# Optimization experiments

Measured on AMD Instinct MI355X. Metric: run time of the kernel, lower is better.

The kernel has to match this reference:

```python
import jax, jax.numpy as jnp
import numpy as np

N_NODES = 100000
N_EDGES = 1600000
N_GRAPHS = 512
IN_F, HID, OUT_F = 50, 128, 4


def _linear_params(key, fan_in, fan_out, bias=True):
    k1, k2 = jax.random.split(key)
    bound = 1.0 / np.sqrt(fan_in)
    W = jax.random.uniform(k1, (fan_out, fan_in), minval=-bound, maxval=bound, dtype=jnp.float32)
    if bias:
        b = jax.random.uniform(k2, (fan_out,), minval=-bound, maxval=bound, dtype=jnp.float32)
        return W, b
    return W, None


def setup_inputs() -> dict:
    key = jax.random.key(0)
    ks = jax.random.split(key, 12)
    x = jax.random.normal(ks[0], (N_NODES, IN_F), dtype=jnp.float32)
    edge_index = jax.random.randint(ks[1], (2, N_EDGES), 0, N_NODES, dtype=jnp.int32)
    batch = jnp.sort(jax.random.randint(ks[2], (N_NODES,), 0, N_GRAPHS, dtype=jnp.int32))
    # GraphConv params: lin_rel (with bias) applied to aggregated msgs, lin_root (no bias)
    W_rel1, b_rel1 = _linear_params(ks[3], IN_F, HID)
    W_root1, _ = _linear_params(ks[4], IN_F, HID, bias=False)
    W_rel2, b_rel2 = _linear_params(ks[5], HID, HID)
    W_root2, _ = _linear_params(ks[6], HID, HID, bias=False)
    W_rel3, b_rel3 = _linear_params(ks[7], HID, HID)
    W_root3, _ = _linear_params(ks[8], HID, HID, bias=False)
    W_lin, b_lin = _linear_params(ks[9], HID, OUT_F)
    return dict(x=x, edge_index=edge_index, batch=batch,
                W_rel1=W_rel1, b_rel1=b_rel1, W_root1=W_root1,
                W_rel2=W_rel2, b_rel2=b_rel2, W_root2=W_root2,
                W_rel3=W_rel3, b_rel3=b_rel3, W_root3=W_root3,
                W_lin=W_lin, b_lin=b_lin)


def _graph_conv(x, src, dst, W_rel, b_rel, W_root):
    # sum-aggregate neighbor features into target nodes, then two linears
    agg = jax.ops.segment_sum(x[src], dst, num_segments=N_NODES)  # [N, F_in]
    return agg @ W_rel.T + b_rel + x @ W_root.T


def reference(x, edge_index, batch,
              W_rel1, b_rel1, W_root1,
              W_rel2, b_rel2, W_root2,
              W_rel3, b_rel3, W_root3,
              W_lin, b_lin):
    src, dst = edge_index[0], edge_index[1]
    h = jax.nn.relu(_graph_conv(x, src, dst, W_rel1, b_rel1, W_root1))
    h = jax.nn.relu(_graph_conv(h, src, dst, W_rel2, b_rel2, W_root2))
    h = _graph_conv(h, src, dst, W_rel3, b_rel3, W_root3)
    # global mean pool over graphs
    sums = jax.ops.segment_sum(h, batch, num_segments=N_GRAPHS)  # [G, HID]
    counts = jax.ops.segment_sum(jnp.ones((N_NODES,), h.dtype), batch, num_segments=N_GRAPHS)
    pooled = sums / jnp.maximum(counts, 1.0)[:, None]
    # dropout is identity in eval mode
    return pooled @ W_lin.T + b_lin
```

## Files before the change

### kernel.cpp

```cpp
#include <hip/hip_runtime.h>
#include <hip/hip_bf16.h>
#include <stdint.h>

#define N_NODES 100000
#define N_EDGES 1600000
#define N_GRAPHS 512
#define IN_F 50
#define HID 128

#define NPART 8
#define PART_NODES ((N_NODES + NPART - 1) / NPART)

typedef __attribute__((ext_vector_type(8))) short bf16x8;
typedef __attribute__((ext_vector_type(4))) float f32x4;

__device__ __forceinline__ float bf2f(unsigned short s) {
    return __uint_as_float(((unsigned)s) << 16);
}
__device__ __forceinline__ unsigned short f2bf(float f) {
    unsigned u = __float_as_uint(f);
    u = (u + 0x7FFFu + ((u >> 16) & 1u)) >> 16;
    return (unsigned short)u;
}

#define PREP_W2 (N_NODES * 64)
#define PREP_W0 N_NODES
#define PREP_W1 (128 * 64 + 128 * 128)
#define PREP_W3 (N_GRAPHS + 1)
#define PREP_TOTAL (PREP_W2 + PREP_W0 + PREP_W1 + PREP_W3)

__global__ __launch_bounds__(256) void prep_all(
    const float* __restrict__ x, unsigned short* __restrict__ xbf,
    int* __restrict__ deg,
    const float* __restrict__ Wr1, const float* __restrict__ Wo1,
    const float* __restrict__ Wr2, const float* __restrict__ Wo2,
    const float* __restrict__ Wr3, const float* __restrict__ Wo3,
    unsigned short* __restrict__ o_r1, unsigned short* __restrict__ o_o1,
    unsigned short* __restrict__ o_r2, unsigned short* __restrict__ o_o2,
    unsigned short* __restrict__ o_r3, unsigned short* __restrict__ o_o3,
    const int* __restrict__ batch, int* __restrict__ gstart) {
    int idx = blockIdx.x * 256 + threadIdx.x;
    if (idx < PREP_W2) {
        int n = idx >> 6, c = idx & 63;
        float v = (c < IN_F) ? x[(size_t)n * IN_F + c] : 0.f;
        xbf[idx] = f2bf(v);
        return;
    }
    idx -= PREP_W2;
    if (idx < PREP_W0) { deg[idx] = 0; return; }
    idx -= PREP_W0;
    if (idx < PREP_W1) {
        if (idx < 128 * 64) {
            int n = idx >> 6, k = idx & 63;
            unsigned short a = 0, b = 0;
            if (k < IN_F) { a = f2bf(Wr1[n * IN_F + k]); b = f2bf(Wo1[n * IN_F + k]); }
            o_r1[idx] = a; o_o1[idx] = b;
        } else {
            int i2 = idx - 128 * 64;
            o_r2[i2] = f2bf(Wr2[i2]); o_o2[i2] = f2bf(Wo2[i2]);
            o_r3[i2] = f2bf(Wr3[i2]); o_o3[i2] = f2bf(Wo3[i2]);
        }
        return;
    }
    idx -= PREP_W1;
    if (idx < PREP_W3) {
        if (idx == N_GRAPHS) { gstart[idx] = N_NODES; return; }
        int lo = 0, hi = N_NODES;
        while (lo < hi) { int m = (lo + hi) >> 1; if (batch[m] < idx) lo = m + 1; else hi = m; }
        gstart[idx] = lo;
    }
}

__global__ __launch_bounds__(256) void deg_hist(const int* __restrict__ dst,
                                                int* __restrict__ deg) {
    int part = blockIdx.x & (NPART - 1);
    int plo = part * PART_NODES, phi = plo + PART_NODES;
    int base = (blockIdx.x >> 3) * 256 + threadIdx.x;
    int stride = (gridDim.x >> 3) * 256;
    for (int e = base; e < N_EDGES; e += stride) {
        int d = dst[e];
        if (d >= plo && d < phi) atomicAdd(&deg[d], 1);
    }
}

__global__ __launch_bounds__(256) void csr_fill(const int* __restrict__ src,
                                                const int* __restrict__ dst,
                                                int* __restrict__ cursor,
                                                int* __restrict__ csr_src) {
    int part = blockIdx.x & (NPART - 1);
    int plo = part * PART_NODES, phi = plo + PART_NODES;
    int base = (blockIdx.x >> 3) * 256 + threadIdx.x;
    int stride = (gridDim.x >> 3) * 256;
    for (int e = base; e < N_EDGES; e += stride) {
        int d = dst[e];
        if (d >= plo && d < phi) {
            int p = atomicAdd(&cursor[d], 1);
            csr_src[p] = src[e];
        }
    }
}

#define SCAN_BLOCKS ((N_NODES + 1023) / 1024)

__global__ __launch_bounds__(256) void scan_phase1(const int* __restrict__ deg,
                                                   int* __restrict__ blocksum) {
    __shared__ int red[256];
    int b = blockIdx.x, t = threadIdx.x;
    int base = b * 1024 + t * 4;
    int s = 0;
#pragma unroll
    for (int i = 0; i < 4; i++) { int idx = base + i; if (idx < N_NODES) s += deg[idx]; }
    red[t] = s;
    __syncthreads();
    for (int off = 128; off > 0; off >>= 1) {
        if (t < off) red[t] += red[t + off];
        __syncthreads();
    }
    if (t == 0) blocksum[b] = red[0];
}

__global__ __launch_bounds__(128) void scan_phase2(const int* __restrict__ blocksum,
                                                   int* __restrict__ blockoff) {
    __shared__ int v[SCAN_BLOCKS];
    int t = threadIdx.x;
    if (t < SCAN_BLOCKS) v[t] = blocksum[t];
    __syncthreads();
    if (t == 0) {
        int run = 0;
        for (int i = 0; i < SCAN_BLOCKS; i++) { blockoff[i] = run; run += v[i]; }
        blockoff[SCAN_BLOCKS] = run;
    }
}

__global__ __launch_bounds__(256) void scan_phase3(const int* __restrict__ deg,
                                                   const int* __restrict__ blockoff,
                                                   int* __restrict__ rowptr,
                                                   int* __restrict__ cursor) {
    __shared__ int red[256];
    int b = blockIdx.x, t = threadIdx.x;
    int base = b * 1024 + t * 4;
    int e[4];
    int s = 0;
#pragma unroll
    for (int i = 0; i < 4; i++) {
        int idx = base + i;
        e[i] = (idx < N_NODES) ? deg[idx] : 0;
        s += e[i];
    }
    red[t] = s;
    __syncthreads();
    for (int off = 1; off < 256; off <<= 1) {
        int u = (t >= off) ? red[t - off] : 0;
        __syncthreads();
        red[t] += u;
        __syncthreads();
    }
    int prefix = red[t] - s + blockoff[b];
#pragma unroll
    for (int i = 0; i < 4; i++) {
        int idx = base + i;
        if (idx < N_NODES) { rowptr[idx] = prefix; cursor[idx] = prefix; prefix += e[i]; }
    }
    if (b == 0 && t == 0) rowptr[N_NODES] = blockoff[SCAN_BLOCKS];
}

__global__ __launch_bounds__(256) void gather_x64(const unsigned short* __restrict__ xbf,
                                                  const int* __restrict__ rowptr,
                                                  const int* __restrict__ csr_src,
                                                  unsigned short* __restrict__ aggbf) {
    int gid = blockIdx.x * 256 + threadIdx.x;
    int n = gid >> 4;
    int c = threadIdx.x & 15;
    if (n >= N_NODES) return;
    int jb = rowptr[n], je = rowptr[n + 1];
    const uint2* hu = reinterpret_cast<const uint2*>(xbf);
    float a0 = 0.f, a1 = 0.f, a2 = 0.f, a3 = 0.f;
    int j = jb;
    for (; j + 3 < je; j += 4) {
        int s0 = csr_src[j], s1 = csr_src[j + 1], s2 = csr_src[j + 2], s3 = csr_src[j + 3];
        uint2 v0 = hu[(size_t)s0 * 16 + c];
        uint2 v1 = hu[(size_t)s1 * 16 + c];
        uint2 v2 = hu[(size_t)s2 * 16 + c];
        uint2 v3 = hu[(size_t)s3 * 16 + c];
        a0 += (bf2f(v0.x & 0xFFFF) + bf2f(v1.x & 0xFFFF)) + (bf2f(v2.x & 0xFFFF) + bf2f(v3.x & 0xFFFF));
        a1 += (bf2f(v0.x >> 16) + bf2f(v1.x >> 16)) + (bf2f(v2.x >> 16) + bf2f(v3.x >> 16));
        a2 += (bf2f(v0.y & 0xFFFF) + bf2f(v1.y & 0xFFFF)) + (bf2f(v2.y & 0xFFFF) + bf2f(v3.y & 0xFFFF));
        a3 += (bf2f(v0.y >> 16) + bf2f(v1.y >> 16)) + (bf2f(v2.y >> 16) + bf2f(v3.y >> 16));
    }
    for (; j < je; j++) {
        int s0 = csr_src[j];
        uint2 v0 = hu[(size_t)s0 * 16 + c];
        a0 += bf2f(v0.x & 0xFFFF);
        a1 += bf2f(v0.x >> 16);
        a2 += bf2f(v0.y & 0xFFFF);
        a3 += bf2f(v0.y >> 16);
    }
    uint2 pk;
    pk.x = (unsigned)f2bf(a0) | ((unsigned)f2bf(a1) << 16);
    pk.y = (unsigned)f2bf(a2) | ((unsigned)f2bf(a3) << 16);
    reinterpret_cast<uint2*>(aggbf)[(size_t)n * 16 + c] = pk;
}

__global__ __launch_bounds__(256) void gather_bf128(const unsigned short* __restrict__ h,
                                                    const int* __restrict__ rowptr,
                                                    const int* __restrict__ csr_src,
                                                    unsigned short* __restrict__ aggbf) {
    int gid = blockIdx.x * 256 + threadIdx.x;
    int n = gid >> 5;
    int c = threadIdx.x & 31;
    if (n >= N_NODES) return;
    int jb = rowptr[n], je = rowptr[n + 1];
    const uint2* hu = reinterpret_cast<const uint2*>(h);
    float a0 = 0.f, a1 = 0.f, a2 = 0.f, a3 = 0.f;
    int j = jb;
    for (; j + 3 < je; j += 4) {
        int s0 = csr_src[j], s1 = csr_src[j + 1], s2 = csr_src[j + 2], s3 = csr_src[j + 3];
        uint2 v0 = hu[(size_t)s0 * 32 + c];
        uint2 v1 = hu[(size_t)s1 * 32 + c];
        uint2 v2 = hu[(size_t)s2 * 32 + c];
        uint2 v3 = hu[(size_t)s3 * 32 + c];
        a0 += (bf2f(v0.x & 0xFFFF) + bf2f(v1.x & 0xFFFF)) + (bf2f(v2.x & 0xFFFF) + bf2f(v3.x & 0xFFFF));
        a1 += (bf2f(v0.x >> 16) + bf2f(v1.x >> 16)) + (bf2f(v2.x >> 16) + bf2f(v3.x >> 16));
        a2 += (bf2f(v0.y & 0xFFFF) + bf2f(v1.y & 0xFFFF)) + (bf2f(v2.y & 0xFFFF) + bf2f(v3.y & 0xFFFF));
        a3 += (bf2f(v0.y >> 16) + bf2f(v1.y >> 16)) + (bf2f(v2.y >> 16) + bf2f(v3.y >> 16));
    }
    for (; j < je; j++) {
        int s0 = csr_src[j];
        uint2 v0 = hu[(size_t)s0 * 32 + c];
        a0 += bf2f(v0.x & 0xFFFF);
        a1 += bf2f(v0.x >> 16);
        a2 += bf2f(v0.y & 0xFFFF);
        a3 += bf2f(v0.y >> 16);
    }
    uint2 pk;
    pk.x = (unsigned)f2bf(a0) | ((unsigned)f2bf(a1) << 16);
    pk.y = (unsigned)f2bf(a2) | ((unsigned)f2bf(a3) << 16);
    reinterpret_cast<uint2*>(aggbf)[(size_t)n * 32 + c] = pk;
}

template <int K1, int K2, bool RELU>
__global__ __launch_bounds__(256) void mfma_linear(
    const unsigned short* __restrict__ A1, const unsigned short* __restrict__ A2,
    const unsigned short* __restrict__ B1, const unsigned short* __restrict__ B2,
    const float* __restrict__ bias, unsigned short* __restrict__ hout) {
    constexpr int P1 = K1 * 2 + 16;
    constexpr int P2 = K2 * 2 + 16;
    constexpr int PMAX = (P1 > P2 ? P1 : P2);
    __shared__ __align__(16) unsigned char ldsb[128 * PMAX];

    const int tid = threadIdx.x;
    const int lane = tid & 63;
    const int wave = tid >> 6;
    const int ar = lane & 15;
    const int kh = lane >> 4;
    const int m0 = blockIdx.x * 128 + wave * 32;

    f32x4 acc0[8], acc1[8];
#pragma unroll
    for (int nt = 0; nt < 8; nt++) {
        acc0[nt] = (f32x4){0.f, 0.f, 0.f, 0.f};
        acc1[nt] = (f32x4){0.f, 0.f, 0.f, 0.f};
    }

    int r0 = m0 + ar;      if (r0 > N_NODES - 1) r0 = N_NODES - 1;
    int r1 = m0 + 16 + ar; if (r1 > N_NODES - 1) r1 = N_NODES - 1;

    {
        constexpr int CPR = K1 / 8;
#pragma unroll
        for (int ci = 0; ci < 128 * CPR / 256; ci++) {
            int c = ci * 256 + tid;
            int n = c / CPR, slot = c - n * CPR;
            uint4 v = *reinterpret_cast<const uint4*>(B1 + n * K1 + slot * 8);
            *reinterpret_cast<uint4*>(&ldsb[n * P1 + slot * 16]) = v;
        }
    }
    __syncthreads();
    {
        const unsigned short* a0p = A1 + (size_t)r0 * K1 + kh * 8;
        const unsigned short* a1p = A1 + (size_t)r1 * K1 + kh * 8;
#pragma unroll
        for (int ks = 0; ks < K1 / 32; ks++) {
            bf16x8 a0 = *reinterpret_cast<const bf16x8*>(a0p + ks * 32);
            bf16x8 a1 = *reinterpret_cast<const bf16x8*>(a1p + ks * 32);
#pragma unroll
            for (int nt = 0; nt < 8; nt++) {
                bf16x8 b = *reinterpret_cast<const bf16x8*>(
                    &ldsb[(nt * 16 + ar) * P1 + ks * 64 + kh * 16]);
                acc0[nt] = __builtin_amdgcn_mfma_f32_16x16x32_bf16(b, a0, acc0[nt], 0, 0, 0);
                acc1[nt] = __builtin_amdgcn_mfma_f32_16x16x32_bf16(b, a1, acc1[nt], 0, 0, 0);
            }
        }
    }
    __syncthreads();
    {
        constexpr int CPR = K2 / 8;
#pragma unroll
        for (int ci = 0; ci < 128 * CPR / 256; ci++) {
            int c = ci * 256 + tid;
            int n = c / CPR, slot = c - n * CPR;
            uint4 v = *reinterpret_cast<const uint4*>(B2 + n * K2 + slot * 8);
            *reinterpret_cast<uint4*>(&ldsb[n * P2 + slot * 16]) = v;
        }
    }
    __syncthreads();
    {
        const unsigned short* a0p = A2 + (size_t)r0 * K2 + kh * 8;
        const unsigned short* a1p = A2 + (size_t)r1 * K2 + kh * 8;
#pragma unroll
        for (int ks = 0; ks < K2 / 32; ks++) {
            bf16x8 a0 = *reinterpret_cast<const bf16x8*>(a0p + ks * 32);
            bf16x8 a1 = *reinterpret_cast<const bf16x8*>(a1p + ks * 32);
#pragma unroll
            for (int nt = 0; nt < 8; nt++) {
                bf16x8 b = *reinterpret_cast<const bf16x8*>(
                    &ldsb[(nt * 16 + ar) * P2 + ks * 64 + kh * 16]);
                acc0[nt] = __builtin_amdgcn_mfma_f32_16x16x32_bf16(b, a0, acc0[nt], 0, 0, 0);
                acc1[nt] = __builtin_amdgcn_mfma_f32_16x16x32_bf16(b, a1, acc1[nt], 0, 0, 0);
            }
        }
    }

    float4 bv[8];
#pragma unroll
    for (int nt = 0; nt < 8; nt++)
        bv[nt] = *reinterpret_cast<const float4*>(bias + nt * 16 + kh * 4);

    int node0 = m0 + ar;
    int node1 = m0 + 16 + ar;
    if (node0 < N_NODES) {
#pragma unroll
        for (int nt = 0; nt < 8; nt++) {
            float v0 = acc0[nt][0] + bv[nt].x;
            float v1 = acc0[nt][1] + bv[nt].y;
            float v2 = acc0[nt][2] + bv[nt].z;
            float v3 = acc0[nt][3] + bv[nt].w;
            if (RELU) { v0 = fmaxf(v0, 0.f); v1 = fmaxf(v1, 0.f); v2 = fmaxf(v2, 0.f); v3 = fmaxf(v3, 0.f); }
            uint2 pk;
            pk.x = (unsigned)f2bf(v0) | ((unsigned)f2bf(v1) << 16);
            pk.y = (unsigned)f2bf(v2) | ((unsigned)f2bf(v3) << 16);
            *reinterpret_cast<uint2*>(hout + (size_t)node0 * HID + nt * 16 + kh * 4) = pk;
        }
    }
    if (node1 < N_NODES) {
#pragma unroll
        for (int nt = 0; nt < 8; nt++) {
            float v0 = acc1[nt][0] + bv[nt].x;
            float v1 = acc1[nt][1] + bv[nt].y;
            float v2 = acc1[nt][2] + bv[nt].z;
            float v3 = acc1[nt][3] + bv[nt].w;
            if (RELU) { v0 = fmaxf(v0, 0.f); v1 = fmaxf(v1, 0.f); v2 = fmaxf(v2, 0.f); v3 = fmaxf(v3, 0.f); }
            uint2 pk;
            pk.x = (unsigned)f2bf(v0) | ((unsigned)f2bf(v1) << 16);
            pk.y = (unsigned)f2bf(v2) | ((unsigned)f2bf(v3) << 16);
            *reinterpret_cast<uint2*>(hout + (size_t)node1 * HID + nt * 16 + kh * 4) = pk;
        }
    }
}

__global__ __launch_bounds__(256) void pool_final(const unsigned short* __restrict__ h3,
                                                  const int* __restrict__ gstart,
                                                  const float* __restrict__ W_lin,
                                                  const float* __restrict__ b_lin,
                                                  float* __restrict__ out) {
    __shared__ float pp[4][HID];
    int g = blockIdx.x, t = threadIdx.x;
    int wave = t >> 6, lane = t & 63;
    int s0 = gstart[g], s1 = gstart[g + 1];
    const unsigned* h3u = reinterpret_cast<const unsigned*>(h3);
    float a0 = 0.f, a1 = 0.f;
    for (int n = s0 + wave; n < s1; n += 4) {
        unsigned v = h3u[(size_t)n * 64 + lane];
        a0 += bf2f((unsigned short)(v & 0xFFFF));
        a1 += bf2f((unsigned short)(v >> 16));
    }
    pp[wave][2 * lane] = a0;
    pp[wave][2 * lane + 1] = a1;
    __syncthreads();
    if (wave == 0) {
        float c = fmaxf((float)(s1 - s0), 1.f);
        float r0 = ((pp[0][2 * lane] + pp[1][2 * lane]) + (pp[2][2 * lane] + pp[3][2 * lane])) / c;
        float r1 = ((pp[0][2 * lane + 1] + pp[1][2 * lane + 1]) + (pp[2][2 * lane + 1] + pp[3][2 * lane + 1])) / c;
        pp[0][2 * lane] = r0;
        pp[0][2 * lane + 1] = r1;
    }
    __syncthreads();
    if (t < 4) {
        float s = b_lin[t];
#pragma unroll 8
        for (int k = 0; k < HID; k++) s += pp[0][k] * W_lin[t * HID + k];
        out[g * 4 + t] = s;
    }
}

extern "C" void kernel_launch(void* const* d_in, const int* in_sizes, int n_in,
                              void* d_out, int out_size, void* d_ws, size_t ws_size,
                              hipStream_t stream) {
    (void)in_sizes; (void)n_in; (void)out_size; (void)ws_size;
    const float* x      = (const float*)d_in[0];
    const int*   ei     = (const int*)d_in[1];
    const int*   batch  = (const int*)d_in[2];
    const float* W_rel1 = (const float*)d_in[3];
    const float* b_rel1 = (const float*)d_in[4];
    const float* W_root1= (const float*)d_in[5];
    const float* W_rel2 = (const float*)d_in[6];
    const float* b_rel2 = (const float*)d_in[7];
    const float* W_root2= (const float*)d_in[8];
    const float* W_rel3 = (const float*)d_in[9];
    const float* b_rel3 = (const float*)d_in[10];
    const float* W_root3= (const float*)d_in[11];
    const float* W_lin  = (const float*)d_in[12];
    const float* b_lin  = (const float*)d_in[13];
    const int* src = ei;
    const int* dst = ei + N_EDGES;

    char* ws = (char*)d_ws;
    size_t off = 0;
    auto alloc = [&](size_t bytes) { void* p = ws + off; off += (bytes + 255) & ~(size_t)255; return p; };
    unsigned short* aggbf    = (unsigned short*)alloc((size_t)N_NODES * HID * 2);
    unsigned short* h1       = (unsigned short*)alloc((size_t)N_NODES * HID * 2);
    unsigned short* xbf      = (unsigned short*)alloc((size_t)N_NODES * 64 * 2);
    int*            deg      = (int*)alloc((size_t)N_NODES * 4);
    int*            rowptr   = (int*)alloc((size_t)(N_NODES + 1) * 4);
    int*            cursor   = (int*)alloc((size_t)N_NODES * 4);
    int*            csr_src  = (int*)alloc((size_t)N_EDGES * 4);
    int*            blocksum = (int*)alloc((size_t)(SCAN_BLOCKS + 1) * 4);
    int*            blockoff = (int*)alloc((size_t)(SCAN_BLOCKS + 1) * 4);
    int*            gstart   = (int*)alloc((size_t)(N_GRAPHS + 1) * 4);
    unsigned short* Wb_rel1  = (unsigned short*)alloc(128 * 64 * 2);
    unsigned short* Wb_root1 = (unsigned short*)alloc(128 * 64 * 2);
    unsigned short* Wb_rel2  = (unsigned short*)alloc(128 * 128 * 2);
    unsigned short* Wb_root2 = (unsigned short*)alloc(128 * 128 * 2);
    unsigned short* Wb_rel3  = (unsigned short*)alloc(128 * 128 * 2);
    unsigned short* Wb_root3 = (unsigned short*)alloc(128 * 128 * 2);

    prep_all<<<(PREP_TOTAL + 255) / 256, 256, 0, stream>>>(
        x, xbf, deg, W_rel1, W_root1, W_rel2, W_root2, W_rel3, W_root3,
        Wb_rel1, Wb_root1, Wb_rel2, Wb_root2, Wb_rel3, Wb_root3, batch, gstart);

    deg_hist<<<2048, 256, 0, stream>>>(dst, deg);
    scan_phase1<<<SCAN_BLOCKS, 256, 0, stream>>>(deg, blocksum);
    scan_phase2<<<1, 128, 0, stream>>>(blocksum, blockoff);
    scan_phase3<<<SCAN_BLOCKS, 256, 0, stream>>>(deg, blockoff, rowptr, cursor);
    csr_fill<<<2048, 256, 0, stream>>>(src, dst, cursor, csr_src);

    const int MFMA_BLOCKS = (N_NODES + 127) / 128;

    gather_x64<<<(N_NODES * 16 + 255) / 256, 256, 0, stream>>>(xbf, rowptr, csr_src, aggbf);
    mfma_linear<64, 64, true><<<MFMA_BLOCKS, 256, 0, stream>>>(
        aggbf, xbf, Wb_rel1, Wb_root1, b_rel1, h1);

    gather_bf128<<<(N_NODES * 32 + 255) / 256, 256, 0, stream>>>(h1, rowptr, csr_src, aggbf);
    mfma_linear<128, 128, true><<<MFMA_BLOCKS, 256, 0, stream>>>(
        aggbf, h1, Wb_rel2, Wb_root2, b_rel2, h1);

    gather_bf128<<<(N_NODES * 32 + 255) / 256, 256, 0, stream>>>(h1, rowptr, csr_src, aggbf);
    mfma_linear<128, 128, false><<<MFMA_BLOCKS, 256, 0, stream>>>(
        aggbf, h1, Wb_rel3, Wb_root3, b_rel3, aggbf);

    pool_final<<<N_GRAPHS, 256, 0, stream>>>(aggbf, gstart, W_lin, b_lin, (float*)d_out);
}
```

Measured before the change: 492.5 us.

## Pre-bucket edges by destination partition before degree histogram and CSR fill

Adds a bucket_scatter pass that splits edges into 8 destination partitions (src,dst pairs) using block-local LDS counters and one global atomic per bucket per block. deg_hist and csr_fill then read only their own partition's pairs instead of every block scanning all edges and filtering by partition. This cuts the 8x redundant reads of dst/src, at the cost of an extra kernel and writing and reading a 12.8 MB pair buffer. BCAP is a fixed per-bucket capacity that assumes a roughly uniform destination distribution.

```diff
diff --git a/kernel.cpp b/kernel.cpp
--- a/kernel.cpp
+++ b/kernel.cpp
@@ -10,6 +10,7 @@
 
 #define NPART 8
 #define PART_NODES ((N_NODES + NPART - 1) / NPART)
+#define BCAP 250000
 
 typedef __attribute__((ext_vector_type(8))) short bf16x8;
 typedef __attribute__((ext_vector_type(4))) float f32x4;
@@ -24,14 +25,14 @@
 }
 
 #define PREP_W2 (N_NODES * 64)
-#define PREP_W0 N_NODES
+#define PREP_W0 (N_NODES + NPART)
 #define PREP_W1 (128 * 64 + 128 * 128)
 #define PREP_W3 (N_GRAPHS + 1)
 #define PREP_TOTAL (PREP_W2 + PREP_W0 + PREP_W1 + PREP_W3)
 
 __global__ __launch_bounds__(256) void prep_all(
     const float* __restrict__ x, unsigned short* __restrict__ xbf,
-    int* __restrict__ deg,
+    int* __restrict__ deg, int* __restrict__ bucket_cnt,
     const float* __restrict__ Wr1, const float* __restrict__ Wo1,
     const float* __restrict__ Wr2, const float* __restrict__ Wo2,
     const float* __restrict__ Wr3, const float* __restrict__ Wo3,
@@ -47,7 +48,11 @@
         return;
     }
     idx -= PREP_W2;
-    if (idx < PREP_W0) { deg[idx] = 0; return; }
+    if (idx < PREP_W0) {
+        if (idx < N_NODES) deg[idx] = 0;
+        else bucket_cnt[idx - N_NODES] = 0;
+        return;
+    }
     idx -= PREP_W0;
     if (idx < PREP_W1) {
         if (idx < 128 * 64) {
@@ -71,32 +76,66 @@
     }
 }
 
-__global__ __launch_bounds__(256) void deg_hist(const int* __restrict__ dst,
+#define B1_BLOCKS 1024
+#define B1_EPT ((N_EDGES + B1_BLOCKS * 256 - 1) / (B1_BLOCKS * 256))
+
+__global__ __launch_bounds__(256) void bucket_scatter(const int* __restrict__ src,
+                                                      const int* __restrict__ dst,
+                                                      int* __restrict__ bucket_cnt,
+                                                      uint2* __restrict__ pairs) {
+    __shared__ int cnt[NPART], base[NPART];
+    int t = threadIdx.x;
+    if (t < NPART) cnt[t] = 0;
+    __syncthreads();
+    const int blockStart = blockIdx.x * (256 * B1_EPT);
+    int dd[B1_EPT], kk[B1_EPT];
+#pragma unroll
+    for (int i = 0; i < B1_EPT; i++) {
+        int e = blockStart + i * 256 + t;
+        int d = (e < N_EDGES) ? dst[e] : -1;
+        dd[i] = d;
+        kk[i] = (d >= 0) ? (d / PART_NODES) : -1;
+        if (kk[i] >= 0) atomicAdd(&cnt[kk[i]], 1);
+    }
+    __syncthreads();
+    if (t < NPART) { base[t] = atomicAdd(&bucket_cnt[t], cnt[t]); cnt[t] = 0; }
+    __syncthreads();
+#pragma unroll
+    for (int i = 0; i < B1_EPT; i++) {
+        int k = kk[i];
+        if (k >= 0) {
+            int e = blockStart + i * 256 + t;
+            int p = base[k] + atomicAdd(&cnt[k], 1);
+            uint2 pr; pr.x = (unsigned)src[e]; pr.y = (unsigned)dd[i];
+            pairs[(size_t)k * BCAP + p] = pr;
+        }
+    }
+}
+
+__global__ __launch_bounds__(256) void deg_hist(const int* __restrict__ bucket_cnt,
+                                                const uint2* __restrict__ pairs,
                                                 int* __restrict__ deg) {
     int part = blockIdx.x & (NPART - 1);
-    int plo = part * PART_NODES, phi = plo + PART_NODES;
+    int cnt = bucket_cnt[part];
+    const uint2* bp = pairs + (size_t)part * BCAP;
     int base = (blockIdx.x >> 3) * 256 + threadIdx.x;
     int stride = (gridDim.x >> 3) * 256;
-    for (int e = base; e < N_EDGES; e += stride) {
-        int d = dst[e];
-        if (d >= plo && d < phi) atomicAdd(&deg[d], 1);
-    }
-}
-
-__global__ __launch_bounds__(256) void csr_fill(const int* __restrict__ src,
-                                                const int* __restrict__ dst,
+    for (int i = base; i < cnt; i += stride) atomicAdd(&deg[bp[i].y], 1);
+}
+
+__global__ __launch_bounds__(256) void csr_fill(const int* __restrict__ bucket_cnt,
+                                                const uint2* __restrict__ pairs,
                                                 int* __restrict__ cursor,
                                                 int* __restrict__ csr_src) {
     int part = blockIdx.x & (NPART - 1);
-    int plo = part * PART_NODES, phi = plo + PART_NODES;
+    int cnt = bucket_cnt[part];
+    const uint2* bp = pairs + (size_t)part * BCAP;
     int base = (blockIdx.x >> 3) * 256 + threadIdx.x;
     int stride = (gridDim.x >> 3) * 256;
-    for (int e = base; e < N_EDGES; e += stride) {
-        int d = dst[e];
-        if (d >= plo && d < phi) {
-            int p = atomicAdd(&cursor[d], 1);
-            csr_src[p] = src[e];
-        }
+    for (int i = base; i < cnt; i += stride) {
+        uint2 pr = bp[i];
+        int p = atomicAdd(&cursor[pr.y], 1);
+        csr_src[p] = (int)pr.x;
     }
 }
 
@@ -424,6 +463,8 @@
     int*            rowptr   = (int*)alloc((size_t)(N_NODES + 1) * 4);
     int*            cursor   = (int*)alloc((size_t)N_NODES * 4);
     int*            csr_src  = (int*)alloc((size_t)N_EDGES * 4);
+    uint2*          pairs    = (uint2*)alloc((size_t)NPART * BCAP * 8);
+    int*            bucket_cnt = (int*)alloc(NPART * 4);
     int*            blocksum = (int*)alloc((size_t)(SCAN_BLOCKS + 1) * 4);
     int*            blockoff = (int*)alloc((size_t)(SCAN_BLOCKS + 1) * 4);
     int*            gstart   = (int*)alloc((size_t)(N_GRAPHS + 1) * 4);
@@ -435,14 +476,15 @@
     unsigned short* Wb_root3 = (unsigned short*)alloc(128 * 128 * 2);
 
     prep_all<<<(PREP_TOTAL + 255) / 256, 256, 0, stream>>>(
-        x, xbf, deg, W_rel1, W_root1, W_rel2, W_root2, W_rel3, W_root3,
+        x, xbf, deg, bucket_cnt, W_rel1, W_root1, W_rel2, W_root2, W_rel3, W_root3,
         Wb_rel1, Wb_root1, Wb_rel2, Wb_root2, Wb_rel3, Wb_root3, batch, gstart);
 
-    deg_hist<<<2048, 256, 0, stream>>>(dst, deg);
+    bucket_scatter<<<B1_BLOCKS, 256, 0, stream>>>(src, dst, bucket_cnt, pairs);
+    deg_hist<<<2048, 256, 0, stream>>>(bucket_cnt, pairs, deg);
     scan_phase1<<<SCAN_BLOCKS, 256, 0, stream>>>(deg, blocksum);
     scan_phase2<<<1, 128, 0, stream>>>(blocksum, blockoff);
     scan_phase3<<<SCAN_BLOCKS, 256, 0, stream>>>(deg, blockoff, rowptr, cursor);
-    csr_fill<<<2048, 256, 0, stream>>>(src, dst, cursor, csr_src);
+    csr_fill<<<2048, 256, 0, stream>>>(bucket_cnt, pairs, cursor, csr_src);
 
     const int MFMA_BLOCKS = (N_NODES + 127) / 128;
 
```

After: 508.1 us. 3.2% more time.

## Build CSR via two-pass bucket scatter and per-partition LDS local sort

Applied to the files above, without the earlier changes.

Replaces the global degree histogram, three-phase scan and atomic-cursor CSR fill with two kernels. The first scatters packed (src, local dst) words into 64 destination buckets using block-local counts. The second builds each partition's rowptr and csr_src with LDS histograms, an in-block scan and LDS cursors. This removes many global atomics and kernel launches. The bucket capacity (BCAP) relies on random edges spreading evenly across partitions, and only 64 blocks run the local sort, so parallelism is limited.

```diff
diff --git a/kernel.cpp b/kernel.cpp
--- a/kernel.cpp
+++ b/kernel.cpp
@@ -8,8 +8,9 @@
 #define IN_F 50
 #define HID 128
 
-#define NPART 8
+#define NPART 64
 #define PART_NODES ((N_NODES + NPART - 1) / NPART)
+#define BCAP 28000
 
 typedef __attribute__((ext_vector_type(8))) short bf16x8;
 typedef __attribute__((ext_vector_type(4))) float f32x4;
@@ -24,14 +25,14 @@
 }
 
 #define PREP_W2 (N_NODES * 64)
-#define PREP_W0 N_NODES
+#define PREP_W0 (NPART + 1)
 #define PREP_W1 (128 * 64 + 128 * 128)
 #define PREP_W3 (N_GRAPHS + 1)
 #define PREP_TOTAL (PREP_W2 + PREP_W0 + PREP_W1 + PREP_W3)
 
 __global__ __launch_bounds__(256) void prep_all(
     const float* __restrict__ x, unsigned short* __restrict__ xbf,
-    int* __restrict__ deg,
+    int* __restrict__ bucket_cnt, int* __restrict__ rowptr,
     const float* __restrict__ Wr1, const float* __restrict__ Wo1,
     const float* __restrict__ Wr2, const float* __restrict__ Wo2,
     const float* __restrict__ Wr3, const float* __restrict__ Wo3,
@@ -47,7 +48,11 @@
         return;
     }
     idx -= PREP_W2;
-    if (idx < PREP_W0) { deg[idx] = 0; return; }
+    if (idx < PREP_W0) {
+        if (idx < NPART) bucket_cnt[idx] = 0;
+        else rowptr[N_NODES] = N_EDGES;
+        return;
+    }
     idx -= PREP_W0;
     if (idx < PREP_W1) {
         if (idx < 128 * 64) {
@@ -71,97 +76,103 @@
     }
 }
 
-__global__ __launch_bounds__(256) void deg_hist(const int* __restrict__ dst,
-                                                int* __restrict__ deg) {
-    int part = blockIdx.x & (NPART - 1);
-    int plo = part * PART_NODES, phi = plo + PART_NODES;
-    int base = (blockIdx.x >> 3) * 256 + threadIdx.x;
-    int stride = (gridDim.x >> 3) * 256;
-    for (int e = base; e < N_EDGES; e += stride) {
-        int d = dst[e];
-        if (d >= plo && d < phi) atomicAdd(&deg[d], 1);
-    }
-}
-
-__global__ __launch_bounds__(256) void csr_fill(const int* __restrict__ src,
-                                                const int* __restrict__ dst,
-                                                int* __restrict__ cursor,
-                                                int* __restrict__ csr_src) {
-    int part = blockIdx.x & (NPART - 1);
-    int plo = part * PART_NODES, phi = plo + PART_NODES;
-    int base = (blockIdx.x >> 3) * 256 + threadIdx.x;
-    int stride = (gridDim.x >> 3) * 256;
-    for (int e = base; e < N_EDGES; e += stride) {
-        int d = dst[e];
-        if (d >= plo && d < phi) {
-            int p = atomicAdd(&cursor[d], 1);
-            csr_src[p] = src[e];
-        }
-    }
-}
-
-#define SCAN_BLOCKS ((N_NODES + 1023) / 1024)
-
-__global__ __launch_bounds__(256) void scan_phase1(const int* __restrict__ deg,
-                                                   int* __restrict__ blocksum) {
-    __shared__ int red[256];
-    int b = blockIdx.x, t = threadIdx.x;
-    int base = b * 1024 + t * 4;
+#define B1_BLOCKS 256
+#define B1_EPT ((N_EDGES + B1_BLOCKS * 256 - 1) / (B1_BLOCKS * 256))
+
+__global__ __launch_bounds__(256) void bucket_scatter(const int* __restrict__ src,
+                                                      const int* __restrict__ dst,
+                                                      int* __restrict__ bucket_cnt,
+                                                      unsigned* __restrict__ pairs) {
+    __shared__ int cnt[NPART], base[NPART];
+    int t = threadIdx.x;
+    for (int i = t; i < NPART; i += 256) cnt[i] = 0;
+    __syncthreads();
+    const int blockStart = blockIdx.x * (256 * B1_EPT);
+    int kk[B1_EPT];
+    unsigned ww[B1_EPT];
+#pragma unroll
+    for (int i = 0; i < B1_EPT; i++) {
+        int e = blockStart + i * 256 + t;
+        if (e < N_EDGES) {
+            int d = dst[e];
+            int k = d / PART_NODES;
+            int local = d - k * PART_NODES;
+            kk[i] = k;
+            ww[i] = ((unsigned)src[e] << 11) | (unsigned)local;
+            atomicAdd(&cnt[k], 1);
+        } else kk[i] = -1;
+    }
+    __syncthreads();
+    for (int i = t; i < NPART; i += 256) { base[i] = atomicAdd(&bucket_cnt[i], cnt[i]); cnt[i] = 0; }
+    __syncthreads();
+#pragma unroll
+    for (int i = 0; i < B1_EPT; i++) {
+        int k = kk[i];
+        if (k >= 0) {
+            int p = base[k] + atomicAdd(&cnt[k], 1);
+            pairs[(size_t)k * BCAP + p] = ww[i];
+        }
+    }
+}
+
+#define LCSR_T 512
+#define LCH ((PART_NODES + LCSR_T - 1) / LCSR_T)
+
+__global__ __launch_bounds__(LCSR_T) void local_csr(const int* __restrict__ bucket_cnt,
+                                                    const unsigned* __restrict__ pairs,
+                                                    int* __restrict__ rowptr,
+                                                    int* __restrict__ csr_src) {
+    __shared__ int cur[PART_NODES];
+    __shared__ int red[LCSR_T];
+    __shared__ int pb[NPART];
+    const int p = blockIdx.x, t = threadIdx.x;
+    const int cnt = bucket_cnt[p];
+    const unsigned* bp = pairs + (size_t)p * BCAP;
+    const int plo = p * PART_NODES;
+
+    for (int i = t; i < PART_NODES; i += LCSR_T) cur[i] = 0;
+    if (t < NPART) pb[t] = bucket_cnt[t];
+    __syncthreads();
+    if (t == 0) {
+        int s = 0;
+        for (int i = 0; i < NPART; i++) { int v = pb[i]; pb[i] = s; s += v; }
+    }
+    for (int i = t; i < cnt; i += LCSR_T) atomicAdd(&cur[bp[i] & 2047u], 1);
+    __syncthreads();
+    const int pbase = pb[p];
+    int e[LCH];
     int s = 0;
 #pragma unroll
-    for (int i = 0; i < 4; i++) { int idx = base + i; if (idx < N_NODES) s += deg[idx]; }
+    for (int i = 0; i < LCH; i++) {
+        int idx = t * LCH + i;
+        e[i] = (idx < PART_NODES) ? cur[idx] : 0;
+        s += e[i];
+    }
     red[t] = s;
     __syncthreads();
-    for (int off = 128; off > 0; off >>= 1) {
-        if (t < off) red[t] += red[t + off];
-        __syncthreads();
-    }
-    if (t == 0) blocksum[b] = red[0];
-}
-
-__global__ __launch_bounds__(128) void scan_phase2(const int* __restrict__ blocksum,
-                                                   int* __restrict__ blockoff) {
-    __shared__ int v[SCAN_BLOCKS];
-    int t = threadIdx.x;
-    if (t < SCAN_BLOCKS) v[t] = blocksum[t];
-    __syncthreads();
-    if (t == 0) {
-        int run = 0;
-        for (int i = 0; i < SCAN_BLOCKS; i++) { blockoff[i] = run; run += v[i]; }
-        blockoff[SCAN_BLOCKS] = run;
-    }
-}
-
-__global__ __launch_bounds__(256) void scan_phase3(const int* __restrict__ deg,
-                                                   const int* __restrict__ blockoff,
-                                                   int* __restrict__ rowptr,
-                                                   int* __restrict__ cursor) {
-    __shared__ int red[256];
-    int b = blockIdx.x, t = threadIdx.x;
-    int base = b * 1024 + t * 4;
-    int e[4];
-    int s = 0;
-#pragma unroll
-    for (int i = 0; i < 4; i++) {
-        int idx = base + i;
-        e[i] = (idx < N_NODES) ? deg[idx] : 0;
-        s += e[i];
-    }
-    red[t] = s;
-    __syncthreads();
-    for (int off = 1; off < 256; off <<= 1) {
-        int u = (t >= off) ? red[t - off] : 0;
+    for (int o = 1; o < LCSR_T; o <<= 1) {
+        int u = (t >= o) ? red[t - o] : 0;
         __syncthreads();
         red[t] += u;
         __syncthreads();
     }
-    int prefix = red[t] - s + blockoff[b];
-#pragma unroll
-    for (int i = 0; i < 4; i++) {
-        int idx = base + i;
-        if (idx < N_NODES) { rowptr[idx] = prefix; cursor[idx] = prefix; prefix += e[i]; }
-    }
-    if (b == 0 && t == 0) rowptr[N_NODES] = blockoff[SCAN_BLOCKS];
+    int run = red[t] - s;
+#pragma unroll
+    for (int i = 0; i < LCH; i++) {
+        int idx = t * LCH + i;
+        if (idx < PART_NODES) {
+            cur[idx] = run;
+            int node = plo + idx;
+            if (node < N_NODES) rowptr[node] = pbase + run;
+            run += e[i];
+        }
+    }
+    __syncthreads();
+    for (int i = t; i < cnt; i += LCSR_T) {
+        unsigned v = bp[i];
+        int pos = pbase + atomicAdd(&cur[v & 2047u], 1);
+        csr_src[pos] = (int)(v >> 11);
+    }
 }
 
 __global__ __launch_bounds__(256) void gather_x64(const unsigned short* __restrict__ xbf,
@@ -420,12 +431,10 @@
     unsigned short* aggbf    = (unsigned short*)alloc((size_t)N_NODES * HID * 2);
     unsigned short* h1       = (unsigned short*)alloc((size_t)N_NODES * HID * 2);
     unsigned short* xbf      = (unsigned short*)alloc((size_t)N_NODES * 64 * 2);
-    int*            deg      = (int*)alloc((size_t)N_NODES * 4);
     int*            rowptr   = (int*)alloc((size_t)(N_NODES + 1) * 4);
-    int*            cursor   = (int*)alloc((size_t)N_NODES * 4);
     int*            csr_src  = (int*)alloc((size_t)N_EDGES * 4);
-    int*            blocksum = (int*)alloc((size_t)(SCAN_BLOCKS + 1) * 4);
-    int*            blockoff = (int*)alloc((size_t)(SCAN_BLOCKS + 1) * 4);
+    unsigned*       pairs    = (unsigned*)alloc((size_t)NPART * BCAP * 4);
+    int*            bucket_cnt = (int*)alloc(NPART * 4);
     int*            gstart   = (int*)alloc((size_t)(N_GRAPHS + 1) * 4);
     unsigned short* Wb_rel1  = (unsigned short*)alloc(128 * 64 * 2);
     unsigned short* Wb_root1 = (unsigned short*)alloc(128 * 64 * 2);
@@ -435,14 +444,11 @@
     unsigned short* Wb_root3 = (unsigned short*)alloc(128 * 128 * 2);
 
     prep_all<<<(PREP_TOTAL + 255) / 256, 256, 0, stream>>>(
-        x, xbf, deg, W_rel1, W_root1, W_rel2, W_root2, W_rel3, W_root3,
+        x, xbf, bucket_cnt, rowptr, W_rel1, W_root1, W_rel2, W_root2, W_rel3, W_root3,
         Wb_rel1, Wb_root1, Wb_rel2, Wb_root2, Wb_rel3, Wb_root3, batch, gstart);
 
-    deg_hist<<<2048, 256, 0, stream>>>(dst, deg);
-    scan_phase1<<<SCAN_BLOCKS, 256, 0, stream>>>(deg, blocksum);
-    scan_phase2<<<1, 128, 0, stream>>>(blocksum, blockoff);
-    scan_phase3<<<SCAN_BLOCKS, 256, 0, stream>>>(deg, blockoff, rowptr, cursor);
-    csr_fill<<<2048, 256, 0, stream>>>(src, dst, cursor, csr_src);
+    bucket_scatter<<<B1_BLOCKS, 256, 0, stream>>>(src, dst, bucket_cnt, pairs);
+    local_csr<<<NPART, LCSR_T, 0, stream>>>(bucket_cnt, pairs, rowptr, csr_src);
 
     const int MFMA_BLOCKS = (N_NODES + 127) / 128;
 
```

Result: faster. 399.6 us (-18.9%).
